# Kernel optimization log

Measured on AMD Instinct MI355X. Metric: run time of the kernel, lower is better.

## Reference

```python
import jax, jax.numpy as jnp
import numpy as np

LAM = 0.3          # margin weight lam (halved inside, as in the torch code)
IGNORE = 255       # ignore_index
NEG = -1e30        # finite -inf stand-in for masking the label class


def setup_inputs() -> dict:
    key = jax.random.key(0)
    k1, k2 = jax.random.split(key)
    logits = jax.random.normal(k1, (8, 19, 512, 512), dtype=jnp.float32)
    labels = jax.random.randint(k2, (8, 512, 512), 0, 19)  # no ignored pixels
    return {"logits": logits, "labels": labels}


def _loss_per_pixel(logits, lb):
    # logits: (N, C, H, W) float32, lb: (N, H, W) int in [0, C)
    C = logits.shape[1]
    coeff = 1.0 / (C - 1.0)
    lam = LAM / 2.0
    onehot = jax.nn.one_hot(lb, C, axis=1, dtype=jnp.bool_)  # (N, C, H, W)
    # softmax over the C-1 non-label classes == softmax with label class masked out
    m_logits = jnp.where(onehot, NEG, logits)
    log_q = jax.nn.log_softmax(m_logits, axis=1)
    q = jnp.exp(log_q)
    margin = jnp.where(onehot, 0.0, (q - coeff) * log_q).sum(axis=1) * lam  # (N, H, W)
    # standard cross-entropy term: -log_softmax(logits)[label]
    log_p = jax.nn.log_softmax(logits, axis=1)
    ce = -jnp.take_along_axis(log_p, lb[:, None], axis=1)[:, 0]  # (N, H, W)
    return margin + ce


def reference(logits, labels):
    valid = labels != IGNORE
    lb = jnp.where(valid, labels, 0)
    loss = _loss_per_pixel(logits.astype(jnp.float32), lb)
    vf = valid.astype(loss.dtype)
    # reduction='mean' over non-ignored pixels
    return (loss * vf).sum() / vf.sum()
```

## Files before the change

kernel.cpp:

```cpp
#include <hip/hip_runtime.h>

#define NCLS 19
#define HW (512 * 512)
#define NPIX (8 * HW)
#define TILE 512
#define NBLK (NPIX / TILE)
#define CHUNKS (NCLS * TILE / 4)

__global__ __launch_bounds__(256) void lms_main_kernel(
    const float* __restrict__ logits, const int* __restrict__ labels,
    float* __restrict__ partials) {
  const float COEFF = 1.0f / 18.0f;
  const float LAM_HALF = 0.15f;

  __shared__ float tile[NCLS * TILE];

  const int t = threadIdx.x;
  const long pixel0 = (long)blockIdx.x * TILE;
  const int n = (int)(pixel0 >> 18);
  const int hw0 = (int)(pixel0 & (HW - 1));
  const float* gbase = logits + (size_t)n * NCLS * HW + hw0;

#pragma unroll
  for (int f = t; f < CHUNKS; f += 256) {
    int r = f >> 7;
    int col = f & 127;
    const float* g = gbase + (size_t)r * HW + col * 4;
    const __attribute__((address_space(1))) float* g1 =
        (const __attribute__((address_space(1))) float*)(uintptr_t)g;
    __attribute__((address_space(3))) float* l3 =
        (__attribute__((address_space(3))) float*)(uintptr_t)(&tile[f * 4]);
    __builtin_amdgcn_global_load_lds(g1, l3, 16, 0, 0);
  }

  int2 lb2 = *(const int2*)(labels + pixel0 + 2 * t);
  int l0 = (lb2.x != 255) ? lb2.x : 0;
  int l1 = (lb2.y != 255) ? lb2.y : 0;

  __syncthreads();

  float s0 = 0.f, T0 = 0.f, S0 = 0.f;
  float s1 = 0.f, T1 = 0.f, S1 = 0.f;
#pragma unroll
  for (int c = 0; c < NCLS; ++c) {
    float2 v = *(const float2*)&tile[c * TILE + 2 * t];
    float e;
    e = __expf(v.x); s0 += e; T0 += e * v.x; S0 += v.x;
    e = __expf(v.y); s1 += e; T1 += e * v.y; S1 += v.y;
  }
  float xl0 = tile[l0 * TILE + 2 * t];
  float xl1 = tile[l1 * TILE + 2 * t + 1];

  float loss = 0.f, cnt = 0.f;
#define PIXEL(s, T, S, xl, lbv)                           \
  {                                                       \
    float el = __expf(xl);                                \
    float sm = s - el;                                    \
    float margin = (T - el * xl) / sm - COEFF * (S - xl); \
    float ce = __logf(s) - xl;                            \
    bool valid = (lbv != 255);                            \
    loss += valid ? (ce + LAM_HALF * margin) : 0.f;       \
    cnt += valid ? 1.f : 0.f;                             \
  }
  PIXEL(s0, T0, S0, xl0, lb2.x)
  PIXEL(s1, T1, S1, xl1, lb2.y)
#undef PIXEL

#pragma unroll
  for (int off = 32; off > 0; off >>= 1) {
    loss += __shfl_down(loss, off, 64);
    cnt += __shfl_down(cnt, off, 64);
  }
  __shared__ float sl[4], sc[4];
  int wave = t >> 6;
  int lane = t & 63;
  if (lane == 0) {
    sl[wave] = loss;
    sc[wave] = cnt;
  }
  __syncthreads();
  if (t == 0) {
    partials[2 * blockIdx.x] = sl[0] + sl[1] + sl[2] + sl[3];
    partials[2 * blockIdx.x + 1] = sc[0] + sc[1] + sc[2] + sc[3];
  }
}

__global__ __launch_bounds__(1024) void lms_final_kernel(
    const float* __restrict__ partials, float* __restrict__ out) {
  int t = threadIdx.x;
  float loss = 0.f, cnt = 0.f;
#pragma unroll
  for (int k = 0; k < 4; ++k) {
    float2 pr = ((const float2*)partials)[t + 1024 * k];
    loss += pr.x;
    cnt += pr.y;
  }
#pragma unroll
  for (int off = 32; off > 0; off >>= 1) {
    loss += __shfl_down(loss, off, 64);
    cnt += __shfl_down(cnt, off, 64);
  }
  __shared__ float sl[16], sc[16];
  int wave = t >> 6;
  int lane = t & 63;
  if (lane == 0) {
    sl[wave] = loss;
    sc[wave] = cnt;
  }
  __syncthreads();
  if (t == 0) {
    float L = 0.f, C = 0.f;
#pragma unroll
    for (int w = 0; w < 16; ++w) {
      L += sl[w];
      C += sc[w];
    }
    out[0] = L / C;
  }
}

extern "C" void kernel_launch(void* const* d_in, const int* in_sizes, int n_in,
                              void* d_out, int out_size, void* d_ws, size_t ws_size,
                              hipStream_t stream) {
  const float* logits = (const float*)d_in[0];
  const int* labels = (const int*)d_in[1];
  float* out = (float*)d_out;
  float* partials = (float*)d_ws;

  lms_main_kernel<<<NBLK, 256, 0, stream>>>(logits, labels, partials);
  lms_final_kernel<<<1, 1024, 0, stream>>>(partials, out);
}
```

Measured before the change: 222.4 us.

## Load logits directly into registers with nontemporal vector loads, 8 pixels per thread

```diff
diff --git a/kernel.cpp b/kernel.cpp
--- a/kernel.cpp
+++ b/kernel.cpp
@@ -3,55 +3,38 @@
 #define NCLS 19
 #define HW (512 * 512)
 #define NPIX (8 * HW)
-#define TILE 512
-#define NBLK (NPIX / TILE)
-#define CHUNKS (NCLS * TILE / 4)
+#define QUADS (NPIX / 4)
+#define NTHREADS (QUADS / 2)
+#define NBLK (NTHREADS / 256)
 
-__global__ __launch_bounds__(256) void lms_main_kernel(
+typedef float vfloat4 __attribute__((ext_vector_type(4)));
+
+__global__ __launch_bounds__(256, 2) void lms_main_kernel(
     const float* __restrict__ logits, const int* __restrict__ labels,
     float* __restrict__ partials) {
   const float COEFF = 1.0f / 18.0f;
   const float LAM_HALF = 0.15f;
 
-  __shared__ float tile[NCLS * TILE];
+  const int t = blockIdx.x * 256 + threadIdx.x;
+  const long pA = (long)t * 4;
+  const long pB = (long)(t + NTHREADS) * 4;
 
-  const int t = threadIdx.x;
-  const long pixel0 = (long)blockIdx.x * TILE;
-  const int n = (int)(pixel0 >> 18);
-  const int hw0 = (int)(pixel0 & (HW - 1));
-  const float* gbase = logits + (size_t)n * NCLS * HW + hw0;
+  const float* baseA = logits + (size_t)(pA >> 18) * NCLS * HW + (int)(pA & (HW - 1));
+  const float* baseB = logits + (size_t)(pB >> 18) * NCLS * HW + (int)(pB & (HW - 1));
 
+  vfloat4 xA[NCLS], xB[NCLS];
 #pragma unroll
-  for (int f = t; f < CHUNKS; f += 256) {
-    int r = f >> 7;
-    int col = f & 127;
-    const float* g = gbase + (size_t)r * HW + col * 4;
-    const __attribute__((address_space(1))) float* g1 =
-        (const __attribute__((address_space(1))) float*)(uintptr_t)g;
-    __attribute__((address_space(3))) float* l3 =
-        (__attribute__((address_space(3))) float*)(uintptr_t)(&tile[f * 4]);
-    __builtin_amdgcn_global_load_lds(g1, l3, 16, 0, 0);
-  }
+  for (int c = 0; c < NCLS; ++c)
+    xA[c] = __builtin_nontemporal_load((const vfloat4*)(baseA + (size_t)c * HW));
+#pragma unroll
+  for (int c = 0; c < NCLS; ++c)
+    xB[c] = __builtin_nontemporal_load((const vfloat4*)(baseB + (size_t)c * HW));
 
-  int2 lb2 = *(const int2*)(labels + pixel0 + 2 * t);
-  int l0 = (lb2.x != 255) ? lb2.x : 0;
-  int l1 = (lb2.y != 255) ? lb2.y : 0;
-
-  __syncthreads();
-
-  float s0 = 0.f, T0 = 0.f, S0 = 0.f;
-  float s1 = 0.f, T1 = 0.f, S1 = 0.f;
-#pragma unroll
-  for (int c = 0; c < NCLS; ++c) {
-    float2 v = *(const float2*)&tile[c * TILE + 2 * t];
-    float e;
-    e = __expf(v.x); s0 += e; T0 += e * v.x; S0 += v.x;
-    e = __expf(v.y); s1 += e; T1 += e * v.y; S1 += v.y;
-  }
-  float xl0 = tile[l0 * TILE + 2 * t];
-  float xl1 = tile[l1 * TILE + 2 * t + 1];
+  int4 lbA = *(const int4*)(labels + pA);
+  int4 lbB = *(const int4*)(labels + pB);
 
   float loss = 0.f, cnt = 0.f;
+
 #define PIXEL(s, T, S, xl, lbv)                           \
   {                                                       \
     float el = __expf(xl);                                \
@@ -62,8 +45,38 @@
     loss += valid ? (ce + LAM_HALF * margin) : 0.f;       \
     cnt += valid ? 1.f : 0.f;                             \
   }
-  PIXEL(s0, T0, S0, xl0, lb2.x)
-  PIXEL(s1, T1, S1, xl1, lb2.y)
+
+#define QUAD(X, LB)                                                \
+  {                                                                \
+    int l0 = (LB.x != 255) ? LB.x : 0;                             \
+    int l1 = (LB.y != 255) ? LB.y : 0;                             \
+    int l2 = (LB.z != 255) ? LB.z : 0;                             \
+    int l3 = (LB.w != 255) ? LB.w : 0;                             \
+    float s0 = 0.f, T0 = 0.f, S0 = 0.f, xl0 = 0.f;                 \
+    float s1 = 0.f, T1 = 0.f, S1 = 0.f, xl1 = 0.f;                 \
+    float s2 = 0.f, T2 = 0.f, S2 = 0.f, xl2 = 0.f;                 \
+    float s3 = 0.f, T3 = 0.f, S3 = 0.f, xl3 = 0.f;                 \
+    _Pragma("unroll") for (int c = 0; c < NCLS; ++c) {             \
+      vfloat4 v = X[c];                                            \
+      float e;                                                     \
+      e = __expf(v.x); s0 += e; T0 += e * v.x; S0 += v.x;          \
+      xl0 = (c == l0) ? v.x : xl0;                                 \
+      e = __expf(v.y); s1 += e; T1 += e * v.y; S1 += v.y;          \
+      xl1 = (c == l1) ? v.y : xl1;                                 \
+      e = __expf(v.z); s2 += e; T2 += e * v.z; S2 += v.z;          \
+      xl2 = (c == l2) ? v.z : xl2;                                 \
+      e = __expf(v.w); s3 += e; T3 += e * v.w; S3 += v.w;          \
+      xl3 = (c == l3) ? v.w : xl3;                                 \
+    }                                                              \
+    PIXEL(s0, T0, S0, xl0, LB.x)                                   \
+    PIXEL(s1, T1, S1, xl1, LB.y)                                   \
+    PIXEL(s2, T2, S2, xl2, LB.z)                                   \
+    PIXEL(s3, T3, S3, xl3, LB.w)                                   \
+  }
+
+  QUAD(xA, lbA)
+  QUAD(xB, lbB)
+#undef QUAD
 #undef PIXEL
 
 #pragma unroll
@@ -72,14 +85,14 @@
     cnt += __shfl_down(cnt, off, 64);
   }
   __shared__ float sl[4], sc[4];
-  int wave = t >> 6;
-  int lane = t & 63;
+  int wave = threadIdx.x >> 6;
+  int lane = threadIdx.x & 63;
   if (lane == 0) {
     sl[wave] = loss;
     sc[wave] = cnt;
   }
   __syncthreads();
-  if (t == 0) {
+  if (threadIdx.x == 0) {
     partials[2 * blockIdx.x] = sl[0] + sl[1] + sl[2] + sl[3];
     partials[2 * blockIdx.x + 1] = sc[0] + sc[1] + sc[2] + sc[3];
   }
@@ -88,13 +101,9 @@
 __global__ __launch_bounds__(1024) void lms_final_kernel(
     const float* __restrict__ partials, float* __restrict__ out) {
   int t = threadIdx.x;
-  float loss = 0.f, cnt = 0.f;
-#pragma unroll
-  for (int k = 0; k < 4; ++k) {
-    float2 pr = ((const float2*)partials)[t + 1024 * k];
-    loss += pr.x;
-    cnt += pr.y;
-  }
+  float2 pr = ((const float2*)partials)[t];
+  float loss = pr.x;
+  float cnt = pr.y;
 #pragma unroll
   for (int off = 32; off > 0; off >>= 1) {
     loss += __shfl_down(loss, off, 64);
```

Result: faster. 214.3 us (-3.7%).
